# Performance work log

Measured on AMD Instinct MI355X. Metric: run time of the kernel, lower is better.

Reference implementation:

```python
import jax, jax.numpy as jnp
import numpy as np

MARGIN = 0.0
GAP = 0.4
N, D, C = 8192, 128, 10


def setup_inputs() -> dict:
    key = jax.random.key(0)
    k1, k2, k3 = jax.random.split(key, 3)
    inputs = jax.random.normal(k1, (N, D), dtype=jnp.float32)
    pred = jax.random.normal(k2, (N, C), dtype=jnp.float32)
    targets = jax.random.randint(k3, (N,), 0, C, dtype=jnp.int64)
    return {"inputs": inputs, "pred": pred, "targets": targets}


def reference(inputs, pred, targets):
    n = inputs.shape[0]
    # pairwise euclidean distances: ||xi||^2 + ||xj||^2 - 2 xi.xj, clamped + sqrt
    sq = jnp.sum(inputs * inputs, axis=1)                      # [n]
    dist = sq[:, None] + sq[None, :] - 2.0 * (inputs @ inputs.T)
    dist = jnp.sqrt(jnp.clip(dist, 1e-12))                     # [n, n]
    same = targets[:, None] == targets[None, :]                # [n, n] bool

    # confusion detection (original runs under no_grad)
    p = jax.nn.softmax(jax.lax.stop_gradient(pred), axis=1)
    val, top2 = jax.lax.top_k(p, 2)                            # [n,2]
    confuse = (val[:, 0] - val[:, 1] <= GAP) | (top2[:, 0] != targets)  # [n]

    # hard mining per row: hardest positive (max over same-class), hardest negative (min over diff-class)
    dist_ap = jnp.max(jnp.where(same, dist, -jnp.inf), axis=1)  # [n]
    dist_an = jnp.min(jnp.where(same, jnp.inf, dist), axis=1)   # [n]

    # MarginRankingLoss(margin=MARGIN) with y=1: mean(relu(-(an - ap) + margin)) over confused rows
    per_row = jnp.maximum(dist_ap - dist_an + MARGIN, 0.0)
    cnt = jnp.sum(confuse.astype(jnp.float32))
    loss = jnp.sum(jnp.where(confuse, per_row, 0.0)) / jnp.maximum(cnt, 1.0)
    return jnp.where(cnt > 0, loss, 0.0)
```

## Files before the change

kernel.cpp:

```cpp
#include <hip/hip_runtime.h>

#define NROWS 8192
#define DIMX  128
#define KB    192
#define KSEG  12
#define PTB   24576
#define NKS   3
#define NCLS  10
#define GAPV  0.4f
#define DEBIAS 504.03125f
#define SCL   (-0.0078125f)
#define RGR   256
#define NRG   (NROWS / RGR)
#define CHUNK 512
#define NCHUNK (NROWS / CHUNK)
#define NT    (CHUNK / 16)

typedef __attribute__((ext_vector_type(4))) int i32x4;

__device__ __forceinline__ int q8(float v) {
  int q = (int)rintf(16.f * v);
  return q > 127 ? 127 : (q < -127 ? -127 : q);
}

__global__ __launch_bounds__(256) void prep_k(const float* __restrict__ x,
                                              const int* __restrict__ tgt,
                                              const float* __restrict__ pred,
                                              char* __restrict__ xa,
                                              char* __restrict__ xbm,
                                              float* __restrict__ sq,
                                              int* __restrict__ conf,
                                              int* __restrict__ emin,
                                              int* __restrict__ emax,
                                              unsigned* __restrict__ ctrs) {
  if (blockIdx.x == 0 && threadIdx.x < 3) ctrs[threadIdx.x] = 0u;
  if (threadIdx.x < 4) {
    const int r = blockIdx.x * 4 + threadIdx.x;
    emin[r] = 0x7FFFFFFF;
    emax[r] = (int)0x80000000;
  }

  const int wave = threadIdx.x >> 6;
  const int lane = threadIdx.x & 63;
  const int row  = blockIdx.x * 4 + wave;
  const float2 f2 = ((const float2*)(x + (size_t)row * DIMX))[lane];
  float s = f2.x * f2.x + f2.y * f2.y;
  #pragma unroll
  for (int m = 1; m < 64; m <<= 1) s += __shfl_xor(s, m, 64);

  char* basea = xa  + (size_t)(row >> 7) * PTB + (size_t)(row & 127) * 16;
  char* baseb = xbm + (size_t)(row >> 7) * PTB + (size_t)(row & 127) * 16;
  {
    const int q0 = q8(f2.x), q1 = q8(f2.y);
    const unsigned short u = (unsigned short)((q0 & 0xFF) | ((q1 & 0xFF) << 8));
    const size_t off = (size_t)(lane >> 3) * 2048 + (lane & 7) * 2;
    *(unsigned short*)(basea + off) = u;
    *(unsigned short*)(baseb + off) = u;
  }
  const int cls = tgt[row];
  if (lane < 32) {
    const int j = 2 * lane;
    unsigned short ua, ub;
    if (lane < 20) {
      const int c = j >> 2;
      const bool hit = (c == cls);
      ua = hit ? (unsigned short)0x7F7F : 0;
      ub = hit ? (unsigned short)0x8181 : 0;
    } else if (lane == 20) {
      const int K = min((int)rintf(128.f * s), 32385);
      const int t = min(K / 127, 254);
      const int b1 = t < 127 ? t : 127;
      const int b2 = t - b1;
      ua = (unsigned short)0x7F7F;
      ub = (unsigned short)(((-b1) & 0xFF) | (((-b2) & 0xFF) << 8));
    } else if (lane == 21) {
      const int K = min((int)rintf(128.f * s), 32385);
      const int t = min(K / 127, 254);
      const int r = min(K - 127 * t, 126);
      ua = (unsigned short)0x0001;
      ub = (unsigned short)((-r) & 0xFF);
    } else { ua = 0; ub = 0; }
    const size_t off = (size_t)(8 + (j >> 4)) * 2048 + (j & 15);
    *(unsigned short*)(basea + off) = ua;
    *(unsigned short*)(baseb + off) = ub;
  }

  if (lane == 0) {
    sq[row] = s;
    const float* pp = pred + (size_t)row * NCLS;
    float v[NCLS];
    #pragma unroll
    for (int c = 0; c < NCLS; ++c) v[c] = pp[c];
    float m1 = v[0]; int i1 = 0;
    #pragma unroll
    for (int c = 1; c < NCLS; ++c)
      if (v[c] > m1) { m1 = v[c]; i1 = c; }
    float m2 = -INFINITY, sum = 0.f;
    #pragma unroll
    for (int c = 0; c < NCLS; ++c) {
      sum += __expf(v[c] - m1);
      if (c != i1) m2 = fmaxf(m2, v[c]);
    }
    const float d01 = (1.f - __expf(m2 - m1)) / sum;
    conf[row] = (d01 <= GAPV) || (i1 != cls);
  }
}

__global__ __launch_bounds__(256)
__attribute__((amdgpu_waves_per_eu(3, 8)))
void gram_k(const char* __restrict__ xa,
            const char* __restrict__ xbm,
            int* __restrict__ emin,
            int* __restrict__ emax) {
  const int tid  = threadIdx.x;
  const int wave = tid >> 6;
  const int lane = tid & 63;
  const int quad = lane >> 4;
  const int m16  = lane & 15;
  const int bx = blockIdx.x, by = blockIdx.y;

  i32x4 A[4][NKS];
  #pragma unroll
  for (int rt = 0; rt < 4; ++rt) {
    const int rbase = wave * 64 + rt * 16;
    const char* pa = xa + (size_t)(bx * 2 + (rbase >> 7)) * PTB
                        + (size_t)((rbase & 127) + m16) * 16;
    #pragma unroll
    for (int ks = 0; ks < NKS; ++ks)
      A[rt][ks] = *(const i32x4*)(pa + (size_t)(ks * 4 + quad) * 2048);
  }
  #pragma unroll
  for (int rt = 0; rt < 4; ++rt)
    #pragma unroll
    for (int ks = 0; ks < NKS; ++ks)
      asm("" : "+v"(A[rt][ks]));

  int Emin[4][4], Emax[4][4];
  #pragma unroll
  for (int r = 0; r < 4; ++r)
    #pragma unroll
    for (int q = 0; q < 4; ++q) { Emin[r][q] = 0x7FFFFFFF; Emax[r][q] = (int)0x80000000; }

  const char* bl = xbm + (size_t)(by * 4) * PTB + (size_t)m16 * 16 + (size_t)quad * 2048;

  i32x4 Bc[NKS], Bn[NKS];
  #pragma unroll
  for (int ks = 0; ks < NKS; ++ks) Bc[ks] = *(const i32x4*)(bl + ks * 8192);

  for (int s = 0; s < NT / 4; ++s) {
    #pragma unroll
    for (int jt = 0; jt < 4; ++jt) {
      const int u  = s * 4 + jt;
      const int un = (u + 1 < NT) ? u + 1 : NT - 1;
      const size_t toff = (size_t)(un >> 3) * PTB + (size_t)(un & 7) * 256;
      #pragma unroll
      for (int ks = 0; ks < NKS; ++ks)
        Bn[ks] = *(const i32x4*)(bl + toff + ks * 8192);

      i32x4 acc[4];
      #pragma unroll
      for (int r = 0; r < 4; ++r) acc[r] = (i32x4){0, 0, 0, 0};
      #pragma unroll
      for (int ks = 0; ks < NKS; ++ks)
        #pragma unroll
        for (int r = 0; r < 4; ++r)
          acc[r] = __builtin_amdgcn_mfma_i32_16x16x64_i8(A[r][ks], Bc[ks], acc[r], 0, 0, 0);

      #pragma unroll
      for (int r = 0; r < 4; ++r)
        #pragma unroll
        for (int q = 0; q < 4; ++q) {
          Emin[r][q] = min(Emin[r][q], acc[r][q]);
          Emax[r][q] = max(Emax[r][q], acc[r][q]);
        }

      #pragma unroll
      for (int ks = 0; ks < NKS; ++ks) Bc[ks] = Bn[ks];
    }
  }

  #pragma unroll
  for (int m = 1; m <= 8; m <<= 1)
    #pragma unroll
    for (int r = 0; r < 4; ++r)
      #pragma unroll
      for (int q = 0; q < 4; ++q) {
        Emin[r][q] = min(Emin[r][q], __shfl_xor(Emin[r][q], m, 64));
        Emax[r][q] = max(Emax[r][q], __shfl_xor(Emax[r][q], m, 64));
      }

  if (m16 == 0) {
    const int rowb = bx * RGR + wave * 64 + quad * 4;
    #pragma unroll
    for (int r = 0; r < 4; ++r)
      #pragma unroll
      for (int q = 0; q < 4; ++q) {
        atomicMin(&emin[rowb + r * 16 + q], Emin[r][q]);
        atomicMax(&emax[rowb + r * 16 + q], Emax[r][q]);
      }
  }
}

__global__ __launch_bounds__(256) void reduce_k(const int* __restrict__ emin,
                                                const int* __restrict__ emax,
                                                const float* __restrict__ sq,
                                                const int* __restrict__ conf,
                                                unsigned* __restrict__ ctrs,
                                                float* __restrict__ out) {
  __shared__ float red[2][4];
  const int tid = threadIdx.x, bx = blockIdx.x;
  const int wave = tid >> 6, lane = tid & 63;
  const int row = bx * RGR + tid;

  unsigned* g_done = ctrs;
  float*    Ssum   = (float*)(ctrs + 1);
  float*    Csum   = (float*)(ctrs + 2);

  const float hi = SCL * (float)emin[row];
  const float lo = SCL * (float)emax[row];
  float ps = 0.f, pc = 0.f;
  if (conf[row]) {
    const float ap = sqrtf(fmaxf(sq[row] + hi - DEBIAS, 1e-12f));
    const float an = sqrtf(fmaxf(sq[row] + lo, 1e-12f));
    ps = fmaxf(ap - an, 0.f);
    pc = 1.f;
  }
  #pragma unroll
  for (int m = 1; m < 64; m <<= 1) {
    ps += __shfl_xor(ps, m, 64);
    pc += __shfl_xor(pc, m, 64);
  }
  if (lane == 0) { red[0][wave] = ps; red[1][wave] = pc; }
  __syncthreads();
  if (tid == 0) {
    atomicAdd(Ssum, red[0][0] + red[0][1] + red[0][2] + red[0][3]);
    atomicAdd(Csum, red[1][0] + red[1][1] + red[1][2] + red[1][3]);
    __threadfence();
    if (atomicAdd(g_done, 1u) == NRG - 1u) {
      const float St = atomicAdd(Ssum, 0.f);
      const float Ct = atomicAdd(Csum, 0.f);
      out[0] = (Ct > 0.f) ? (St / fmaxf(Ct, 1.f)) : 0.f;
    }
  }
}

extern "C" void kernel_launch(void* const* d_in, const int* in_sizes, int n_in,
                              void* d_out, int out_size, void* d_ws, size_t ws_size,
                              hipStream_t stream) {
  const float* x    = (const float*)d_in[0];
  const float* pred = (const float*)d_in[1];
  const int*   tgt  = (const int*)d_in[2];
  float* out = (float*)d_out;

  char* w = (char*)d_ws;
  const size_t arr_bytes = (size_t)NROWS * KB;
  char*  xa   = w;
  char*  xbm  = w + arr_bytes;
  float* sq   = (float*)(w + 2 * arr_bytes);
  int*   conf = (int*)(w + 2 * arr_bytes + (size_t)NROWS * 4);
  int*   emin = (int*)(w + 2 * arr_bytes + (size_t)NROWS * 8);
  int*   emax = (int*)(w + 2 * arr_bytes + (size_t)NROWS * 12);
  unsigned* ctrs = (unsigned*)(w + 2 * arr_bytes + (size_t)NROWS * 16);

  hipLaunchKernelGGL(prep_k, dim3(NROWS / 4), dim3(256), 0, stream,
                     x, tgt, pred, xa, xbm, sq, conf, emin, emax, ctrs);
  hipLaunchKernelGGL(gram_k, dim3(NRG, NCHUNK), dim3(256), 0, stream,
                     xa, xbm, emin, emax);
  hipLaunchKernelGGL(reduce_k, dim3(NRG), dim3(256), 0, stream,
                     emin, emax, sq, conf, ctrs, out);
}
```

Before: 83.10 us.

## Fuse final reduction into gram kernel via last-block pattern and pair min/max updates

Removes the separate reduce kernel: each gram block increments a global counter, and the last block to finish reads all emin/emax rows and computes the final loss. The min/max update is now done once per two tiles, using two alternating accumulator sets. The waves-per-EU hint is relaxed from 3 to 2 to leave room for the extra registers. This saves one launch, at the cost of a serial 8192-row reduction in a single block and possible lower occupancy.

```diff
diff --git a/kernel.cpp b/kernel.cpp
--- a/kernel.cpp
+++ b/kernel.cpp
@@ -15,6 +15,7 @@
 #define CHUNK 512
 #define NCHUNK (NROWS / CHUNK)
 #define NT    (CHUNK / 16)
+#define NBLK  (NRG * NCHUNK)
 
 typedef __attribute__((ext_vector_type(4))) int i32x4;
 
@@ -107,11 +108,17 @@
 }
 
 __global__ __launch_bounds__(256)
-__attribute__((amdgpu_waves_per_eu(3, 8)))
+__attribute__((amdgpu_waves_per_eu(2, 8)))
 void gram_k(const char* __restrict__ xa,
             const char* __restrict__ xbm,
+            const float* __restrict__ sq,
+            const int* __restrict__ conf,
             int* __restrict__ emin,
-            int* __restrict__ emax) {
+            int* __restrict__ emax,
+            unsigned* __restrict__ ctrs,
+            float* __restrict__ out) {
+  __shared__ float red[2][4];
+  __shared__ unsigned last_flag;
   const int tid  = threadIdx.x;
   const int wave = tid >> 6;
   const int lane = tid & 63;
@@ -147,6 +154,7 @@
   #pragma unroll
   for (int ks = 0; ks < NKS; ++ks) Bc[ks] = *(const i32x4*)(bl + ks * 8192);
 
+  i32x4 accA[4], accB[4];
   for (int s = 0; s < NT / 4; ++s) {
     #pragma unroll
     for (int jt = 0; jt < 4; ++jt) {
@@ -157,7 +165,7 @@
       for (int ks = 0; ks < NKS; ++ks)
         Bn[ks] = *(const i32x4*)(bl + toff + ks * 8192);
 
-      i32x4 acc[4];
+      i32x4 (&acc)[4] = (jt & 1) ? accB : accA;
       #pragma unroll
       for (int r = 0; r < 4; ++r) acc[r] = (i32x4){0, 0, 0, 0};
       #pragma unroll
@@ -166,13 +174,15 @@
         for (int r = 0; r < 4; ++r)
           acc[r] = __builtin_amdgcn_mfma_i32_16x16x64_i8(A[r][ks], Bc[ks], acc[r], 0, 0, 0);
 
-      #pragma unroll
-      for (int r = 0; r < 4; ++r)
+      if (jt & 1) {
         #pragma unroll
-        for (int q = 0; q < 4; ++q) {
-          Emin[r][q] = min(Emin[r][q], acc[r][q]);
-          Emax[r][q] = max(Emax[r][q], acc[r][q]);
-        }
+        for (int r = 0; r < 4; ++r)
+          #pragma unroll
+          for (int q = 0; q < 4; ++q) {
+            Emin[r][q] = min(Emin[r][q], min(accA[r][q], accB[r][q]));
+            Emax[r][q] = max(Emax[r][q], max(accA[r][q], accB[r][q]));
+          }
+      }
 
       #pragma unroll
       for (int ks = 0; ks < NKS; ++ks) Bc[ks] = Bn[ks];
@@ -199,46 +209,35 @@
         atomicMax(&emax[rowb + r * 16 + q], Emax[r][q]);
       }
   }
-}
-
-__global__ __launch_bounds__(256) void reduce_k(const int* __restrict__ emin,
-                                                const int* __restrict__ emax,
-                                                const float* __restrict__ sq,
-                                                const int* __restrict__ conf,
-                                                unsigned* __restrict__ ctrs,
-                                                float* __restrict__ out) {
-  __shared__ float red[2][4];
-  const int tid = threadIdx.x, bx = blockIdx.x;
-  const int wave = tid >> 6, lane = tid & 63;
-  const int row = bx * RGR + tid;
-
-  unsigned* g_done = ctrs;
-  float*    Ssum   = (float*)(ctrs + 1);
-  float*    Csum   = (float*)(ctrs + 2);
-
-  const float hi = SCL * (float)emin[row];
-  const float lo = SCL * (float)emax[row];
-  float ps = 0.f, pc = 0.f;
-  if (conf[row]) {
-    const float ap = sqrtf(fmaxf(sq[row] + hi - DEBIAS, 1e-12f));
-    const float an = sqrtf(fmaxf(sq[row] + lo, 1e-12f));
-    ps = fmaxf(ap - an, 0.f);
-    pc = 1.f;
-  }
-  #pragma unroll
-  for (int m = 1; m < 64; m <<= 1) {
-    ps += __shfl_xor(ps, m, 64);
-    pc += __shfl_xor(pc, m, 64);
-  }
-  if (lane == 0) { red[0][wave] = ps; red[1][wave] = pc; }
+
+  asm volatile("s_waitcnt vmcnt(0)" ::: "memory");
   __syncthreads();
-  if (tid == 0) {
-    atomicAdd(Ssum, red[0][0] + red[0][1] + red[0][2] + red[0][3]);
-    atomicAdd(Csum, red[1][0] + red[1][1] + red[1][2] + red[1][3]);
-    __threadfence();
-    if (atomicAdd(g_done, 1u) == NRG - 1u) {
-      const float St = atomicAdd(Ssum, 0.f);
-      const float Ct = atomicAdd(Csum, 0.f);
+  if (tid == 0) last_flag = (atomicAdd(&ctrs[0], 1u) == NBLK - 1u) ? 1u : 0u;
+  __syncthreads();
+  if (last_flag) {
+    float ps = 0.f, pc = 0.f;
+    #pragma unroll
+    for (int i = 0; i < NROWS / 256; ++i) {
+      const int row = i * 256 + tid;
+      const int lo = atomicAdd(&emin[row], 0);
+      const int hi = atomicAdd(&emax[row], 0);
+      if (conf[row]) {
+        const float ap = sqrtf(fmaxf(sq[row] + SCL * (float)lo - DEBIAS, 1e-12f));
+        const float an = sqrtf(fmaxf(sq[row] + SCL * (float)hi, 1e-12f));
+        ps += fmaxf(ap - an, 0.f);
+        pc += 1.f;
+      }
+    }
+    #pragma unroll
+    for (int m = 1; m < 64; m <<= 1) {
+      ps += __shfl_xor(ps, m, 64);
+      pc += __shfl_xor(pc, m, 64);
+    }
+    if (lane == 0) { red[0][wave] = ps; red[1][wave] = pc; }
+    __syncthreads();
+    if (tid == 0) {
+      const float St = red[0][0] + red[0][1] + red[0][2] + red[0][3];
+      const float Ct = red[1][0] + red[1][1] + red[1][2] + red[1][3];
       out[0] = (Ct > 0.f) ? (St / fmaxf(Ct, 1.f)) : 0.f;
     }
   }
@@ -265,7 +264,5 @@
   hipLaunchKernelGGL(prep_k, dim3(NROWS / 4), dim3(256), 0, stream,
                      x, tgt, pred, xa, xbm, sq, conf, emin, emax, ctrs);
   hipLaunchKernelGGL(gram_k, dim3(NRG, NCHUNK), dim3(256), 0, stream,
-                     xa, xbm, emin, emax);
-  hipLaunchKernelGGL(reduce_k, dim3(NRG), dim3(256), 0, stream,
-                     emin, emax, sq, conf, ctrs, out);
-}
+                     xa, xbm, sq, conf, emin, emax, ctrs, out);
+}
```

Measured after the change: 103.8 us. 1.25x slower.

## Quantize A operand inside gram kernel and halve rows per block

Applied to the files above, without the earlier changes.

Drops the separate xa quantized buffer. The gram kernel now reads fp32 rows of x directly, quantizes them to int8 in registers and builds the class/bias columns from the targets itself. Rows per block go from 256 to 128, doubling the grid in x, and the prep kernel processes 8 rows per wave with 8x fewer blocks. This cuts workspace writes and traffic in prep, but gram blocks now re-read fp32 x, and twice as many blocks stream the B operand, which adds reload traffic.

```diff
diff --git a/kernel.cpp b/kernel.cpp
--- a/kernel.cpp
+++ b/kernel.cpp
@@ -3,14 +3,13 @@
 #define NROWS 8192
 #define DIMX  128
 #define KB    192
-#define KSEG  12
 #define PTB   24576
 #define NKS   3
 #define NCLS  10
 #define GAPV  0.4f
 #define DEBIAS 504.03125f
 #define SCL   (-0.0078125f)
-#define RGR   256
+#define RGR   128
 #define NRG   (NROWS / RGR)
 #define CHUNK 512
 #define NCHUNK (NROWS / CHUNK)
@@ -22,11 +21,14 @@
   int q = (int)rintf(16.f * v);
   return q > 127 ? 127 : (q < -127 ? -127 : q);
 }
+__device__ __forceinline__ int pk4(float4 v) {
+  return (q8(v.x) & 255) | ((q8(v.y) & 255) << 8) |
+         ((q8(v.z) & 255) << 16) | ((q8(v.w) & 255) << 24);
+}
 
 __global__ __launch_bounds__(256) void prep_k(const float* __restrict__ x,
                                               const int* __restrict__ tgt,
                                               const float* __restrict__ pred,
-                                              char* __restrict__ xa,
                                               char* __restrict__ xbm,
                                               float* __restrict__ sq,
                                               int* __restrict__ conf,
@@ -34,81 +36,77 @@
                                               int* __restrict__ emax,
                                               unsigned* __restrict__ ctrs) {
   if (blockIdx.x == 0 && threadIdx.x < 3) ctrs[threadIdx.x] = 0u;
-  if (threadIdx.x < 4) {
-    const int r = blockIdx.x * 4 + threadIdx.x;
+  if (threadIdx.x < 32) {
+    const int r = blockIdx.x * 32 + threadIdx.x;
     emin[r] = 0x7FFFFFFF;
     emax[r] = (int)0x80000000;
   }
 
   const int wave = threadIdx.x >> 6;
   const int lane = threadIdx.x & 63;
-  const int row  = blockIdx.x * 4 + wave;
-  const float2 f2 = ((const float2*)(x + (size_t)row * DIMX))[lane];
-  float s = f2.x * f2.x + f2.y * f2.y;
-  #pragma unroll
-  for (int m = 1; m < 64; m <<= 1) s += __shfl_xor(s, m, 64);
-
-  char* basea = xa  + (size_t)(row >> 7) * PTB + (size_t)(row & 127) * 16;
-  char* baseb = xbm + (size_t)(row >> 7) * PTB + (size_t)(row & 127) * 16;
-  {
-    const int q0 = q8(f2.x), q1 = q8(f2.y);
-    const unsigned short u = (unsigned short)((q0 & 0xFF) | ((q1 & 0xFF) << 8));
-    const size_t off = (size_t)(lane >> 3) * 2048 + (lane & 7) * 2;
-    *(unsigned short*)(basea + off) = u;
-    *(unsigned short*)(baseb + off) = u;
-  }
-  const int cls = tgt[row];
-  if (lane < 32) {
-    const int j = 2 * lane;
-    unsigned short ua, ub;
-    if (lane < 20) {
-      const int c = j >> 2;
-      const bool hit = (c == cls);
-      ua = hit ? (unsigned short)0x7F7F : 0;
-      ub = hit ? (unsigned short)0x8181 : 0;
-    } else if (lane == 20) {
-      const int K = min((int)rintf(128.f * s), 32385);
-      const int t = min(K / 127, 254);
-      const int b1 = t < 127 ? t : 127;
-      const int b2 = t - b1;
-      ua = (unsigned short)0x7F7F;
-      ub = (unsigned short)(((-b1) & 0xFF) | (((-b2) & 0xFF) << 8));
-    } else if (lane == 21) {
-      const int K = min((int)rintf(128.f * s), 32385);
-      const int t = min(K / 127, 254);
-      const int r = min(K - 127 * t, 126);
-      ua = (unsigned short)0x0001;
-      ub = (unsigned short)((-r) & 0xFF);
-    } else { ua = 0; ub = 0; }
-    const size_t off = (size_t)(8 + (j >> 4)) * 2048 + (j & 15);
-    *(unsigned short*)(basea + off) = ua;
-    *(unsigned short*)(baseb + off) = ub;
-  }
-
-  if (lane == 0) {
-    sq[row] = s;
-    const float* pp = pred + (size_t)row * NCLS;
-    float v[NCLS];
-    #pragma unroll
-    for (int c = 0; c < NCLS; ++c) v[c] = pp[c];
-    float m1 = v[0]; int i1 = 0;
-    #pragma unroll
-    for (int c = 1; c < NCLS; ++c)
-      if (v[c] > m1) { m1 = v[c]; i1 = c; }
-    float m2 = -INFINITY, sum = 0.f;
-    #pragma unroll
-    for (int c = 0; c < NCLS; ++c) {
-      sum += __expf(v[c] - m1);
-      if (c != i1) m2 = fmaxf(m2, v[c]);
-    }
-    const float d01 = (1.f - __expf(m2 - m1)) / sum;
-    conf[row] = (d01 <= GAPV) || (i1 != cls);
+
+  for (int r8 = 0; r8 < 8; ++r8) {
+    const int row = blockIdx.x * 32 + r8 * 4 + wave;
+    const float2 f2 = ((const float2*)(x + (size_t)row * DIMX))[lane];
+    float s = f2.x * f2.x + f2.y * f2.y;
+    #pragma unroll
+    for (int m = 1; m < 64; m <<= 1) s += __shfl_xor(s, m, 64);
+
+    char* baseb = xbm + (size_t)(row >> 7) * PTB + (size_t)(row & 127) * 16;
+    {
+      const int q0 = q8(f2.x), q1 = q8(f2.y);
+      const unsigned short u = (unsigned short)((q0 & 0xFF) | ((q1 & 0xFF) << 8));
+      const size_t off = (size_t)(lane >> 3) * 2048 + (lane & 7) * 2;
+      *(unsigned short*)(baseb + off) = u;
+    }
+    const int cls = tgt[row];
+    if (lane < 32) {
+      const int j = 2 * lane;
+      unsigned short ub;
+      if (lane < 20) {
+        ub = ((j >> 2) == cls) ? (unsigned short)0x8181 : 0;
+      } else if (lane == 20) {
+        const int K = min((int)rintf(128.f * s), 32385);
+        const int t = min(K / 127, 254);
+        const int b1 = t < 127 ? t : 127;
+        const int b2 = t - b1;
+        ub = (unsigned short)(((-b1) & 0xFF) | (((-b2) & 0xFF) << 8));
+      } else if (lane == 21) {
+        const int K = min((int)rintf(128.f * s), 32385);
+        const int t = min(K / 127, 254);
+        const int r = min(K - 127 * t, 126);
+        ub = (unsigned short)((-r) & 0xFF);
+      } else ub = 0;
+      const size_t off = (size_t)(8 + (j >> 4)) * 2048 + (j & 15);
+      *(unsigned short*)(baseb + off) = ub;
+    }
+
+    if (lane == 0) {
+      sq[row] = s;
+      const float* pp = pred + (size_t)row * NCLS;
+      float v[NCLS];
+      #pragma unroll
+      for (int c = 0; c < NCLS; ++c) v[c] = pp[c];
+      float m1 = v[0]; int i1 = 0;
+      #pragma unroll
+      for (int c = 1; c < NCLS; ++c)
+        if (v[c] > m1) { m1 = v[c]; i1 = c; }
+      float m2 = -INFINITY, sum = 0.f;
+      #pragma unroll
+      for (int c = 0; c < NCLS; ++c) {
+        sum += __expf(v[c] - m1);
+        if (c != i1) m2 = fmaxf(m2, v[c]);
+      }
+      const float d01 = (1.f - __expf(m2 - m1)) / sum;
+      conf[row] = (d01 <= GAPV) || (i1 != cls);
+    }
   }
 }
 
 __global__ __launch_bounds__(256)
-__attribute__((amdgpu_waves_per_eu(3, 8)))
-void gram_k(const char* __restrict__ xa,
+__attribute__((amdgpu_waves_per_eu(2, 8)))
+void gram_k(const float* __restrict__ x,
+            const int* __restrict__ tgt,
             const char* __restrict__ xbm,
             int* __restrict__ emin,
             int* __restrict__ emax) {
@@ -119,25 +117,34 @@
   const int m16  = lane & 15;
   const int bx = blockIdx.x, by = blockIdx.y;
 
-  i32x4 A[4][NKS];
-  #pragma unroll
-  for (int rt = 0; rt < 4; ++rt) {
-    const int rbase = wave * 64 + rt * 16;
-    const char* pa = xa + (size_t)(bx * 2 + (rbase >> 7)) * PTB
-                        + (size_t)((rbase & 127) + m16) * 16;
-    #pragma unroll
-    for (int ks = 0; ks < NKS; ++ks)
-      A[rt][ks] = *(const i32x4*)(pa + (size_t)(ks * 4 + quad) * 2048);
-  }
-  #pragma unroll
-  for (int rt = 0; rt < 4; ++rt)
+  i32x4 A[2][NKS];
+  #pragma unroll
+  for (int rt = 0; rt < 2; ++rt) {
+    const int row = bx * RGR + wave * 32 + rt * 16 + m16;
+    const float4* xr = (const float4*)(x + (size_t)row * DIMX);
+    #pragma unroll
+    for (int ks = 0; ks < 2; ++ks) {
+      const float4* p = xr + ks * 16 + quad * 4;
+      i32x4 f;
+      #pragma unroll
+      for (int w = 0; w < 4; ++w) f[w] = pk4(p[w]);
+      A[rt][ks] = f;
+    }
+    const int cls = tgt[row];
+    i32x4 a2 = {0, 0, 0, 0};
+    if ((cls >> 2) == quad) a2[cls & 3] = 0x7F7F7F7F;
+    if (quad == 2) a2[2] |= 0x00017F7F;
+    A[rt][2] = a2;
+  }
+  #pragma unroll
+  for (int rt = 0; rt < 2; ++rt)
     #pragma unroll
     for (int ks = 0; ks < NKS; ++ks)
       asm("" : "+v"(A[rt][ks]));
 
-  int Emin[4][4], Emax[4][4];
-  #pragma unroll
-  for (int r = 0; r < 4; ++r)
+  int Emin[2][4], Emax[2][4];
+  #pragma unroll
+  for (int r = 0; r < 2; ++r)
     #pragma unroll
     for (int q = 0; q < 4; ++q) { Emin[r][q] = 0x7FFFFFFF; Emax[r][q] = (int)0x80000000; }
 
@@ -157,17 +164,17 @@
       for (int ks = 0; ks < NKS; ++ks)
         Bn[ks] = *(const i32x4*)(bl + toff + ks * 8192);
 
-      i32x4 acc[4];
-      #pragma unroll
-      for (int r = 0; r < 4; ++r) acc[r] = (i32x4){0, 0, 0, 0};
+      i32x4 acc[2];
+      #pragma unroll
+      for (int r = 0; r < 2; ++r) acc[r] = (i32x4){0, 0, 0, 0};
       #pragma unroll
       for (int ks = 0; ks < NKS; ++ks)
         #pragma unroll
-        for (int r = 0; r < 4; ++r)
+        for (int r = 0; r < 2; ++r)
           acc[r] = __builtin_amdgcn_mfma_i32_16x16x64_i8(A[r][ks], Bc[ks], acc[r], 0, 0, 0);
 
       #pragma unroll
-      for (int r = 0; r < 4; ++r)
+      for (int r = 0; r < 2; ++r)
         #pragma unroll
         for (int q = 0; q < 4; ++q) {
           Emin[r][q] = min(Emin[r][q], acc[r][q]);
@@ -182,7 +189,7 @@
   #pragma unroll
   for (int m = 1; m <= 8; m <<= 1)
     #pragma unroll
-    for (int r = 0; r < 4; ++r)
+    for (int r = 0; r < 2; ++r)
       #pragma unroll
       for (int q = 0; q < 4; ++q) {
         Emin[r][q] = min(Emin[r][q], __shfl_xor(Emin[r][q], m, 64));
@@ -190,9 +197,9 @@
       }
 
   if (m16 == 0) {
-    const int rowb = bx * RGR + wave * 64 + quad * 4;
-    #pragma unroll
-    for (int r = 0; r < 4; ++r)
+    const int rowb = bx * RGR + wave * 32 + quad * 4;
+    #pragma unroll
+    for (int r = 0; r < 2; ++r)
       #pragma unroll
       for (int q = 0; q < 4; ++q) {
         atomicMin(&emin[rowb + r * 16 + q], Emin[r][q]);
@@ -210,7 +217,7 @@
   __shared__ float red[2][4];
   const int tid = threadIdx.x, bx = blockIdx.x;
   const int wave = tid >> 6, lane = tid & 63;
-  const int row = bx * RGR + tid;
+  const int row = bx * 256 + tid;
 
   unsigned* g_done = ctrs;
   float*    Ssum   = (float*)(ctrs + 1);
@@ -236,7 +243,7 @@
     atomicAdd(Ssum, red[0][0] + red[0][1] + red[0][2] + red[0][3]);
     atomicAdd(Csum, red[1][0] + red[1][1] + red[1][2] + red[1][3]);
     __threadfence();
-    if (atomicAdd(g_done, 1u) == NRG - 1u) {
+    if (atomicAdd(g_done, 1u) == 31u) {
       const float St = atomicAdd(Ssum, 0.f);
       const float Ct = atomicAdd(Csum, 0.f);
       out[0] = (Ct > 0.f) ? (St / fmaxf(Ct, 1.f)) : 0.f;
@@ -254,18 +261,17 @@
 
   char* w = (char*)d_ws;
   const size_t arr_bytes = (size_t)NROWS * KB;
-  char*  xa   = w;
-  char*  xbm  = w + arr_bytes;
-  float* sq   = (float*)(w + 2 * arr_bytes);
-  int*   conf = (int*)(w + 2 * arr_bytes + (size_t)NROWS * 4);
-  int*   emin = (int*)(w + 2 * arr_bytes + (size_t)NROWS * 8);
-  int*   emax = (int*)(w + 2 * arr_bytes + (size_t)NROWS * 12);
-  unsigned* ctrs = (unsigned*)(w + 2 * arr_bytes + (size_t)NROWS * 16);
-
-  hipLaunchKernelGGL(prep_k, dim3(NROWS / 4), dim3(256), 0, stream,
-                     x, tgt, pred, xa, xbm, sq, conf, emin, emax, ctrs);
+  char*  xbm  = w;
+  float* sq   = (float*)(w + arr_bytes);
+  int*   conf = (int*)(w + arr_bytes + (size_t)NROWS * 4);
+  int*   emin = (int*)(w + arr_bytes + (size_t)NROWS * 8);
+  int*   emax = (int*)(w + arr_bytes + (size_t)NROWS * 12);
+  unsigned* ctrs = (unsigned*)(w + arr_bytes + (size_t)NROWS * 16);
+
+  hipLaunchKernelGGL(prep_k, dim3(NROWS / 32), dim3(256), 0, stream,
+                     x, tgt, pred, xbm, sq, conf, emin, emax, ctrs);
   hipLaunchKernelGGL(gram_k, dim3(NRG, NCHUNK), dim3(256), 0, stream,
-                     xa, xbm, emin, emax);
-  hipLaunchKernelGGL(reduce_k, dim3(NRG), dim3(256), 0, stream,
+                     x, tgt, xbm, emin, emax);
+  hipLaunchKernelGGL(reduce_k, dim3(32), dim3(256), 0, stream,
                      emin, emax, sq, conf, ctrs, out);
 }
```

After: 96.26 us. 1.16x slower.
